# Optimization experiments

Measured on AMD Instinct MI355X. Metric: run time of the kernel, lower is better.

Reference implementation:

```python
import jax, jax.numpy as jnp
import numpy as np
from jax import lax


def setup_inputs() -> dict:
    key = jax.random.key(0)
    k1, k2, k3 = jax.random.split(key, 3)
    B, Ci, Co, K, H, W = 8, 512, 512, 3, 32, 32
    x = jax.random.normal(k1, (B, Ci, H, W), dtype=jnp.float32)
    y_s = jax.random.normal(k2, (B, Ci), dtype=jnp.float32)
    weight = jax.random.normal(k3, (Co, Ci, K, K), dtype=jnp.float32)  # scale_init = 1 (equal_lr)
    bias = jnp.zeros((Co,), dtype=jnp.float32)
    return {"x": x, "y_s": y_s, "weight": weight, "bias": bias}


def reference(x, y_s, weight, bias):
    # equal_lr=True -> runtime scale = (in_channels * k^2) ** -0.5
    Co, Ci, K, _ = weight.shape
    scale_forward = (Ci * K * K) ** -0.5
    w = scale_forward * weight  # [Co, Ci, K, K]

    # Fused StyleGAN2 trick (mathematically identical to per-sample grouped conv):
    # conv(x, y_s[b,i]*w[o,i]) == conv(x * y_s, w); demod divides by per-(b,o) norm.
    x_mod = x * y_s[:, :, None, None]
    out = lax.conv_general_dilated(
        x_mod, w,
        window_strides=(1, 1),
        padding=((1, 1), (1, 1)),
        rhs_dilation=(1, 1),
        dimension_numbers=("NCHW", "OIHW", "NCHW"),
    )  # [B, Co, H, W]

    # demod=True: x_s[b,o] = sqrt(sum_{i,kh,kw} (y_s[b,i]*w[o,i,kh,kw])^2 + 1e-8)
    w2 = jnp.sum(w * w, axis=(2, 3))  # [Co, Ci]
    xs = jnp.sqrt(jnp.einsum("bi,oi->bo", y_s * y_s, w2) + 1e-8)  # [B, Co]
    out = out / xs[:, :, None, None] + bias[None, :, None, None]
    return out
```

## Files before the change

kernel.cpp:

```cpp
#include <hip/hip_runtime.h>

typedef __attribute__((ext_vector_type(8))) short short8;
typedef __attribute__((ext_vector_type(4))) float f32x4;

#define RCP_OFF   0
#define WPRE_OFF  16384
#define XM_OFF    4734976

__device__ __forceinline__ unsigned short f2bf(float f) {
  unsigned int u = __float_as_uint(f);
  u += 0x7FFFu + ((u >> 16) & 1u);
  return (unsigned short)(u >> 16);
}

__device__ __forceinline__ void gload_lds16(const void* g, void* l) {
  __builtin_amdgcn_global_load_lds(
      (__attribute__((address_space(1))) void*)g,
      (__attribute__((address_space(3))) void*)l, 16, 0, 0);
}

__global__ __launch_bounds__(256) void prep_kernel(
    const float* __restrict__ x, const float* __restrict__ ys,
    const float* __restrict__ w,
    unsigned short* __restrict__ xm, unsigned short* __restrict__ wpre,
    float* __restrict__ rcp) {
  int bid = blockIdx.x;
  int tid = threadIdx.x;

  if (bid < 512) {
    int half = bid & 1;
    int h = (bid >> 1) & 31;
    int b = bid >> 6;
    __shared__ float tile[256][33];
    int ci0 = half * 256;
#pragma unroll
    for (int r = 0; r < 32; ++r) {
      int ci = r * 8 + (tid >> 5);
      int wcol = tid & 31;
      float v = x[(((size_t)b * 512 + ci0 + ci) * 32 + h) * 32 + wcol];
      tile[ci][wcol] = v * ys[b * 512 + ci0 + ci];
    }
    __syncthreads();
    int g0 = half * 32;
    for (int r = 0; r < 5; ++r) {
      int idx = r * 256 + tid;
      if (idx < 1088) {
        int gl = idx / 34;
        int col = idx - gl * 34;
        short8 v = {0,0,0,0,0,0,0,0};
        if (col != 0 && col != 33) {
          int wcol = col - 1;
#pragma unroll
          for (int j = 0; j < 8; ++j)
            v[j] = (short)f2bf(tile[gl * 8 + j][wcol]);
        }
        size_t off = ((((size_t)b * 64 + g0 + gl) * 34 + (h + 1)) * 34 + col) * 8;
        *reinterpret_cast<short8*>(xm + off) = v;
      }
    }
    if (h == 0 || h == 31) {
      int hp = (h == 0) ? 0 : 33;
      for (int r = 0; r < 5; ++r) {
        int idx = r * 256 + tid;
        if (idx < 1088) {
          int gl = idx / 34;
          int col = idx - gl * 34;
          short8 z = {0,0,0,0,0,0,0,0};
          size_t off = ((((size_t)b * 64 + g0 + gl) * 34 + hp) * 34 + col) * 8;
          *reinterpret_cast<short8*>(xm + off) = z;
        }
      }
    }
  } else if (bid < 640) {
    int pid = bid - 512;
    int coh = pid & 1;
    int kb = (pid >> 1) & 7;
    int c = pid >> 4;
    int co = coh * 256 + tid;
    int ci0 = c * 64 + kb * 8;
    const float* wp = w + (size_t)co * 4608 + (size_t)ci0 * 9;
    float v[72];
    const f32x4* wp4 = reinterpret_cast<const f32x4*>(wp);
#pragma unroll
    for (int i = 0; i < 18; ++i) {
      f32x4 q = wp4[i];
      v[i * 4 + 0] = q[0]; v[i * 4 + 1] = q[1]; v[i * 4 + 2] = q[2]; v[i * 4 + 3] = q[3];
    }
    const float scale = 1.4731391274719738e-02f;
#pragma unroll
    for (int t = 0; t < 9; ++t) {
      short8 s;
#pragma unroll
      for (int j = 0; j < 8; ++j) s[j] = (short)f2bf(scale * v[j * 9 + t]);
      *reinterpret_cast<short8*>(wpre + ((((size_t)c * 9 + t) * 8 + kb) * 512 + co) * 8) = s;
    }
  } else {
    int pid = bid - 640;
    int wv = tid >> 6;
    int lane = tid & 63;
    int o = pid * 4 + wv;
    const float* wp = w + (size_t)o * 4608 + (size_t)lane * 72;
    const float scale2 = 1.0f / 4608.0f;
    float w2[8];
#pragma unroll
    for (int j = 0; j < 8; ++j) {
      float s = 0.f;
#pragma unroll
      for (int k = 0; k < 9; ++k) { float vv = wp[j * 9 + k]; s += vv * vv; }
      w2[j] = s * scale2;
    }
#pragma unroll
    for (int b = 0; b < 8; ++b) {
      float p = 0.f;
#pragma unroll
      for (int j = 0; j < 8; ++j) {
        float y = ys[b * 512 + lane * 8 + j];
        p += y * y * w2[j];
      }
#pragma unroll
      for (int off = 32; off > 0; off >>= 1) p += __shfl_down(p, off);
      if (lane == 0) rcp[b * 512 + o] = 1.0f / sqrtf(p + 1e-8f);
    }
  }
}

__global__ __launch_bounds__(512, 1) void conv_main(
    const unsigned short* __restrict__ wpre,
    const unsigned short* __restrict__ xm,
    const float* __restrict__ rcp,
    const float* __restrict__ bias,
    float* __restrict__ out)
{
  __shared__ __align__(16) char smem[52224];

  int bid = blockIdx.x;
  int xcd = bid & 7;
  int j0 = bid >> 3;
  int cog = xcd >> 1;
  int sp = (xcd & 1) * 32 + j0;
  int b = sp >> 3;
  int hg = sp & 7;
  int tid = threadIdx.x;
  int lane = tid & 63;
  int wv = tid >> 6;
  int wc = wv & 1;
  int wr = (wv >> 1) & 1;
  int kp = wv >> 2;
  int l15 = lane & 15, l4 = lane >> 4;

  f32x4 acc[4][4];
#pragma unroll
  for (int i = 0; i < 4; ++i)
#pragma unroll
    for (int jj = 0; jj < 4; ++jj) { f32x4 z = {0.f,0.f,0.f,0.f}; acc[i][jj] = z; }

  const unsigned short* xmb = xm + (size_t)b * (64 * 34 * 34 * 8);
  const unsigned short* wbase =
      wpre + ((size_t)(kp * 4 + l4) * 512 + cog * 128 + wr * 64 + l15) * 8;
  const int bbase = (kp * 4 + l4) * 3264 + wc * 2 * 544 + l15 * 16;

  int soff_[4], sld_[4];
  bool sact_[4];
#pragma unroll
  for (int p = 0; p < 4; ++p) {
    int idx = p * 512 + tid;
    sact_[p] = idx < 1632;
    int kb = idx / 204;
    int rem = idx - kb * 204;
    int rr = rem / 34;
    int col = rem - rr * 34;
    soff_[p] = ((kb * 34 + hg * 4 + rr) * 34 + col) * 8;
    sld_[p] = idx * 16;
  }

  auto stageX = [&](int c, int buf) {
    char* xb = smem + buf * 26112;
    const unsigned short* base = xmb + (size_t)c * 73984;
#pragma unroll
    for (int p = 0; p < 4; ++p)
      if (sact_[p]) gload_lds16(base + soff_[p], xb + sld_[p]);
  };

  auto loadA = [&](int ct, short8 (&a)[4]) {
    const unsigned short* p = wbase + (size_t)ct * 32768;
#pragma unroll
    for (int mi = 0; mi < 4; ++mi)
      a[mi] = *reinterpret_cast<const short8*>(p + mi * 128);
  };

  auto loadB = [&](const char* xb, int t, short8 (&f)[4]) {
    int kh = t / 3, kw = t % 3;
#pragma unroll
    for (int nj = 0; nj < 4; ++nj) {
      int imm = ((nj >> 1) + kh) * 544 + (nj & 1) * 256 + kw * 16;
      f[nj] = *reinterpret_cast<const short8*>(xb + bbase + imm);
    }
  };

  short8 X[4], Y[4], Z[4];

  stageX(0, 0);
  loadA(0, X);
  loadA(1, Y);
  asm volatile("s_waitcnt vmcnt(8)" ::: "memory");
  __builtin_amdgcn_s_barrier();
  asm volatile("" ::: "memory");

  for (int c = 0; c < 8; ++c) {
    const char* xb = smem + (c & 1) * 26112;
    short8 Bp[4], Bq[4];
    loadB(xb, 0, Bp);
#pragma unroll
    for (int t = 0; t < 9; ++t) {
      int ct = c * 9 + t;
      short8 (&curA)[4] = (t % 3 == 0) ? X : ((t % 3 == 1) ? Y : Z);
      short8 (&nxtA)[4] = (t % 3 == 0) ? Z : ((t % 3 == 1) ? X : Y);
      short8 (&curB)[4] = (t & 1) ? Bq : Bp;
      short8 (&nxtB)[4] = (t & 1) ? Bp : Bq;
      if (ct < 70) loadA(ct + 2, nxtA);
      if (t == 4 && c < 7)
        stageX(c + 1, (c + 1) & 1);
      __builtin_amdgcn_s_barrier();
      asm volatile("s_waitcnt lgkmcnt(0)" ::: "memory");
      __builtin_amdgcn_sched_barrier(0);
      if (t < 8) loadB(xb, t + 1, nxtB);
      __builtin_amdgcn_s_setprio(1);
#pragma unroll
      for (int nj = 0; nj < 4; ++nj)
#pragma unroll
        for (int mi = 0; mi < 4; ++mi)
          acc[mi][nj] = __builtin_amdgcn_mfma_f32_16x16x32_bf16(curA[mi], curB[nj], acc[mi][nj], 0, 0, 0);
      __builtin_amdgcn_s_setprio(0);
    }
    if (c < 7) {
      asm volatile("s_waitcnt vmcnt(8) lgkmcnt(0)" ::: "memory");
      __builtin_amdgcn_s_barrier();
      asm volatile("" ::: "memory");
    }
  }
  __syncthreads();

#pragma unroll
  for (int p = 0; p < 2; ++p) {
    if (kp == 1 && wr == p) {
#pragma unroll
      for (int mi = 0; mi < 4; ++mi)
#pragma unroll
        for (int nj = 0; nj < 4; ++nj)
          *reinterpret_cast<f32x4*>(smem + wc * 16384 + (mi * 4 + nj) * 1024 + lane * 16) = acc[mi][nj];
    }
    __syncthreads();
    if (kp == 0 && wr == p) {
#pragma unroll
      for (int mi = 0; mi < 4; ++mi)
#pragma unroll
        for (int nj = 0; nj < 4; ++nj) {
          f32x4 v = *reinterpret_cast<const f32x4*>(smem + wc * 16384 + (mi * 4 + nj) * 1024 + lane * 16);
          acc[mi][nj] = acc[mi][nj] + v;
        }
    }
    __syncthreads();
  }

  if (kp == 0) {
    const float* rcpb = rcp + b * 512;
#pragma unroll
    for (int mi = 0; mi < 4; ++mi) {
      int ob = cog * 128 + wr * 64 + mi * 16 + l4 * 4;
      float rc[4], bi[4];
#pragma unroll
      for (int jj = 0; jj < 4; ++jj) { rc[jj] = rcpb[ob + jj]; bi[jj] = bias[ob + jj]; }
#pragma unroll
      for (int nj = 0; nj < 4; ++nj) {
        int row4 = wc * 2 + (nj >> 1);
        int wcol = (nj & 1) * 16 + l15;
        int h = hg * 4 + row4;
#pragma unroll
        for (int jj = 0; jj < 4; ++jj)
          out[(((size_t)b * 512 + ob + jj) * 32 + h) * 32 + wcol] = acc[mi][nj][jj] * rc[jj] + bi[jj];
      }
    }
  }
}

extern "C" void kernel_launch(void* const* d_in, const int* in_sizes, int n_in,
                              void* d_out, int out_size, void* d_ws, size_t ws_size,
                              hipStream_t stream) {
  const float* x    = (const float*)d_in[0];
  const float* ys   = (const float*)d_in[1];
  const float* w    = (const float*)d_in[2];
  const float* bias = (const float*)d_in[3];
  float* out = (float*)d_out;
  char* ws = (char*)d_ws;
  float* rcp = (float*)(ws + RCP_OFF);
  unsigned short* wpre = (unsigned short*)(ws + WPRE_OFF);
  unsigned short* xm   = (unsigned short*)(ws + XM_OFF);

  prep_kernel<<<768, 256, 0, stream>>>(x, ys, w, xm, wpre, rcp);
  conv_main<<<256, 512, 0, stream>>>(wpre, xm, rcp, bias, out);
}
```

Measured before the change: 55.03 us.

## Batch LDS B-fragment loads per kernel row to cut barriers per chunk

The inner loop over the nine 3x3 taps is restructured into three groups of three taps (one per kernel row). Each group loads twelve B fragments from LDS at once, double-buffered across rows. This cuts the block barriers and lgkmcnt waits per channel chunk from nine to three, so more MFMAs run between synchronisations. In exchange it needs many more VGPRs for B fragments, which could lower occupancy or cause spills, and the prefetch of the next X chunk moves to a different point in the loop.

```diff
diff --git a/kernel.cpp b/kernel.cpp
--- a/kernel.cpp
+++ b/kernel.cpp
@@ -188,13 +188,14 @@
       a[mi] = *reinterpret_cast<const short8*>(p + mi * 128);
   };
 
-  auto loadB = [&](const char* xb, int t, short8 (&f)[4]) {
-    int kh = t / 3, kw = t % 3;
-#pragma unroll
-    for (int nj = 0; nj < 4; ++nj) {
-      int imm = ((nj >> 1) + kh) * 544 + (nj & 1) * 256 + kw * 16;
-      f[nj] = *reinterpret_cast<const short8*>(xb + bbase + imm);
-    }
+  auto loadB3 = [&](const char* xb, int kh, short8 (&f)[12]) {
+#pragma unroll
+    for (int kw = 0; kw < 3; ++kw)
+#pragma unroll
+      for (int nj = 0; nj < 4; ++nj) {
+        int imm = ((nj >> 1) + kh) * 544 + (nj & 1) * 256 + kw * 16;
+        f[kw * 4 + nj] = *reinterpret_cast<const short8*>(xb + bbase + imm);
+      }
   };
 
   short8 X[4], Y[4], Z[4];
@@ -208,28 +209,32 @@
 
   for (int c = 0; c < 8; ++c) {
     const char* xb = smem + (c & 1) * 26112;
-    short8 Bp[4], Bq[4];
-    loadB(xb, 0, Bp);
-#pragma unroll
-    for (int t = 0; t < 9; ++t) {
-      int ct = c * 9 + t;
-      short8 (&curA)[4] = (t % 3 == 0) ? X : ((t % 3 == 1) ? Y : Z);
-      short8 (&nxtA)[4] = (t % 3 == 0) ? Z : ((t % 3 == 1) ? X : Y);
-      short8 (&curB)[4] = (t & 1) ? Bq : Bp;
-      short8 (&nxtB)[4] = (t & 1) ? Bp : Bq;
-      if (ct < 70) loadA(ct + 2, nxtA);
-      if (t == 4 && c < 7)
-        stageX(c + 1, (c + 1) & 1);
+    short8 P[12], Q[12];
+    loadB3(xb, 0, P);
+#pragma unroll
+    for (int tp = 0; tp < 3; ++tp) {
       __builtin_amdgcn_s_barrier();
       asm volatile("s_waitcnt lgkmcnt(0)" ::: "memory");
       __builtin_amdgcn_sched_barrier(0);
-      if (t < 8) loadB(xb, t + 1, nxtB);
+      if (tp == 1 && c < 7)
+        stageX(c + 1, (c + 1) & 1);
+      short8 (&curB)[12] = (tp == 1) ? Q : P;
+      short8 (&nxtB)[12] = (tp == 1) ? P : Q;
+      if (tp < 2) loadB3(xb, tp + 1, nxtB);
       __builtin_amdgcn_s_setprio(1);
 #pragma unroll
-      for (int nj = 0; nj < 4; ++nj)
-#pragma unroll
-        for (int mi = 0; mi < 4; ++mi)
-          acc[mi][nj] = __builtin_amdgcn_mfma_f32_16x16x32_bf16(curA[mi], curB[nj], acc[mi][nj], 0, 0, 0);
+      for (int tt = 0; tt < 3; ++tt) {
+        int ct = c * 9 + tp * 3 + tt;
+        short8 (&curA)[4] = (tt == 0) ? X : ((tt == 1) ? Y : Z);
+        short8 (&nxtA)[4] = (tt == 0) ? Z : ((tt == 1) ? X : Y);
+        if (ct < 70) loadA(ct + 2, nxtA);
+#pragma unroll
+        for (int nj = 0; nj < 4; ++nj)
+#pragma unroll
+          for (int mi = 0; mi < 4; ++mi)
+            acc[mi][nj] = __builtin_amdgcn_mfma_f32_16x16x32_bf16(
+                curA[mi], curB[tt * 4 + nj], acc[mi][nj], 0, 0, 0);
+      }
       __builtin_amdgcn_s_setprio(0);
     }
     if (c < 7) {
```

Result: slower. 57.99 us (+5.4%).
